# Kernel tuning notes

Measured on AMD Instinct MI355X. Metric: run time of the kernel, lower is better.

Reference implementation:

```python
import math
import jax, jax.numpy as jnp
import numpy as np

B, S, H, E, F = 4, 2048, 1024, 8, 2048
CAPACITY_FACTOR = 1.25


def setup_inputs() -> dict:
    key = jax.random.key(0)
    ks = jax.random.split(key, 5)
    x = jax.random.normal(ks[0], (B, S, H), dtype=jnp.float32)
    gate_w = jax.random.normal(ks[1], (H, E), dtype=jnp.float32) * 0.02
    w1 = jax.random.normal(ks[2], (E, H, F), dtype=jnp.float32) * 0.02
    w2 = jax.random.normal(ks[3], (E, F, H), dtype=jnp.float32) * 0.02
    w3 = jax.random.normal(ks[4], (E, H, F), dtype=jnp.float32) * 0.02
    return {"x": x, "gate_w": gate_w, "w1": w1, "w2": w2, "w3": w3}


def reference(x, gate_w, w1, w2, w3):
    b, s, h = x.shape
    T = b * s
    e = gate_w.shape[1]
    xf = x.reshape(T, h)                           # [T, H]
    logits = xf @ gate_w                           # [T, E]
    capacity = min(math.ceil(T / e * CAPACITY_FACTOR), T)
    # Expert-choice: each expert picks its top-`capacity` tokens.
    scores, idx = jax.lax.top_k(logits.T, capacity)  # both [E, C]
    # Per-expert softmax over the selected tokens (dim=0 of the column vector in torch == capacity axis here).
    weights = jax.nn.softmax(scores, axis=1)       # [E, C]
    gathered = xf[idx]                             # [E, C, H]
    # Grouped SwiGLU FFN
    a = jnp.einsum('ech,ehf->ecf', gathered, w1)
    g = jnp.einsum('ech,ehf->ecf', gathered, w3)
    hidden = jax.nn.silu(a) * g                    # [E, C, F]
    out_e = jnp.einsum('ecf,efh->ech', hidden, w2) # [E, C, H]
    out_e = out_e * weights[..., None]
    # Weighted scatter-add combine
    yf = jnp.zeros((T, h), dtype=x.dtype).at[idx.reshape(-1)].add(
        out_e.reshape(-1, h))
    return yf.reshape(b, s, h), jnp.float32(0.0)
```

## Files before the change

### kernel.cpp

```cpp
#include <hip/hip_runtime.h>
#include <stdint.h>

typedef unsigned short ushort_t;
typedef __bf16 bf16x8 __attribute__((ext_vector_type(8)));
typedef float f32x4 __attribute__((ext_vector_type(4)));

#define T_TOK 8192
#define HDIM  1024
#define EXP   8
#define FDIM  2048
#define CAP   1280

__device__ __forceinline__ unsigned short f2b(float f) {
  unsigned u = __float_as_uint(f);
  u = (u + 0x7fffu + ((u >> 16) & 1u)) >> 16;
  return (unsigned short)u;
}
__device__ __forceinline__ unsigned pk2(unsigned short lo, unsigned short hi) {
  return (unsigned)lo | ((unsigned)hi << 16);
}
__device__ __forceinline__ unsigned map_u(float f) {
  unsigned u = __float_as_uint(f);
  return (u & 0x80000000u) ? ~u : (u | 0x80000000u);
}
__device__ __forceinline__ float unmap_f(unsigned m) {
  unsigned u = (m & 0x80000000u) ? (m ^ 0x80000000u) : ~m;
  return __uint_as_float(u);
}
__device__ __forceinline__ void gl_lds16(const void* g, void* l) {
  __builtin_amdgcn_global_load_lds((__attribute__((address_space(1))) void*)g,
                                   (__attribute__((address_space(3))) void*)l,
                                   16, 0, 0);
}

__global__ void __launch_bounds__(256) gate_cast_k(
    const float* __restrict__ x, const float* __restrict__ gw,
    float* __restrict__ logitsT, ushort_t* __restrict__ xb)
{
  int wave = threadIdx.x >> 6, lane = threadIdx.x & 63;
  int t = blockIdx.x * 4 + wave;
  const float* xr = x + (size_t)t * HDIM;
  ushort_t* xbr = xb + (size_t)t * HDIM;
  float acc[8];
#pragma unroll
  for (int i = 0; i < 8; ++i) acc[i] = 0.f;
#pragma unroll
  for (int i = 0; i < 16; ++i) {
    int h = i * 64 + lane;
    float xv = xr[h];
    xbr[h] = f2b(xv);
    const float4* g4 = (const float4*)(gw + (size_t)h * EXP);
    float4 lo = g4[0], hi = g4[1];
    acc[0] += xv * lo.x; acc[1] += xv * lo.y; acc[2] += xv * lo.z; acc[3] += xv * lo.w;
    acc[4] += xv * hi.x; acc[5] += xv * hi.y; acc[6] += xv * hi.z; acc[7] += xv * hi.w;
  }
#pragma unroll
  for (int off = 32; off > 0; off >>= 1) {
#pragma unroll
    for (int i = 0; i < 8; ++i) acc[i] += __shfl_xor(acc[i], off, 64);
  }
  if (lane == 0) {
#pragma unroll
    for (int i = 0; i < 8; ++i) logitsT[(size_t)i * T_TOK + t] = acc[i];
  }
}

__global__ void __launch_bounds__(256) select_k(
    const float* __restrict__ logitsT,
    unsigned* __restrict__ thr, int* __restrict__ needo, unsigned* __restrict__ umax)
{
  __shared__ int hist[256];
  __shared__ int ssum[256];
  __shared__ unsigned s_pref;
  __shared__ int s_rem;
  __shared__ unsigned smx[4];
  int e = blockIdx.x, tid = threadIdx.x;
  const float* base = logitsT + (size_t)e * T_TOK;

  unsigned m[32];
  unsigned mmax = 0;
#pragma unroll
  for (int i = 0; i < 32; ++i) {
    m[i] = map_u(base[tid + i * 256]);
    mmax = m[i] > mmax ? m[i] : mmax;
  }
#pragma unroll
  for (int off = 32; off > 0; off >>= 1) {
    unsigned o = __shfl_xor(mmax, off, 64);
    mmax = o > mmax ? o : mmax;
  }
  int lane = tid & 63, wv = tid >> 6;
  if (lane == 0) smx[wv] = mmax;
  if (tid == 0) { s_pref = 0; s_rem = CAP; }
  __syncthreads();
  if (tid == 0) {
    unsigned a = smx[0] > smx[1] ? smx[0] : smx[1];
    unsigned b = smx[2] > smx[3] ? smx[2] : smx[3];
    umax[e] = a > b ? a : b;
  }

  for (int r = 0; r < 4; ++r) {
    hist[tid] = 0;
    __syncthreads();
    unsigned pref = s_pref;
    int rem = s_rem;
    int shift = 24 - 8 * r;
#pragma unroll
    for (int i = 0; i < 32; ++i) {
      unsigned u = m[i];
      bool ok = (r == 0) || ((u >> (shift + 8)) == (pref >> (shift + 8)));
      if (ok) atomicAdd(&hist[(u >> shift) & 255], 1);
    }
    __syncthreads();
    ssum[tid] = hist[tid];
    __syncthreads();
    for (int st = 1; st < 256; st <<= 1) {
      int add = (tid + st < 256) ? ssum[tid + st] : 0;
      __syncthreads();
      ssum[tid] += add;
      __syncthreads();
    }
    int above = (tid < 255) ? ssum[tid + 1] : 0;
    if (ssum[tid] >= rem && above < rem) {
      s_pref = pref | ((unsigned)tid << shift);
      s_rem = rem - above;
    }
    __syncthreads();
  }
  if (tid == 0) { thr[e] = s_pref; needo[e] = s_rem; }
}

__global__ void __launch_bounds__(256) emit_k(
    const float* __restrict__ logitsT,
    const unsigned* __restrict__ thr, const int* __restrict__ needv,
    const unsigned* __restrict__ umaxv,
    int* __restrict__ idxo, float* __restrict__ exo,
    int* __restrict__ cnt, int* __restrict__ tie, float* __restrict__ expsum,
    int* __restrict__ tok_cnt, int* __restrict__ tok_ent)
{
  int t = blockIdx.x * 256 + threadIdx.x;
  int lane = threadIdx.x & 63;
  int lc = 0;
  int ents[8];
#pragma unroll
  for (int e = 0; e < EXP; ++e) {
    float f = logitsT[(size_t)e * T_TOK + t];
    unsigned u = map_u(f);
    unsigned te = thr[e];
    float fm = unmap_f(umaxv[e]);
    float v = __expf(f - fm);
    bool sel = u > te;
    unsigned long long mask = __ballot(sel);
    int nsel = __popcll(mask);
    int base = 0;
    if (lane == 0 && nsel) base = atomicAdd(&cnt[e], nsel);
    base = __shfl(base, 0, 64);
    int slot = -1;
    if (sel) slot = base + __popcll(mask & ((1ull << lane) - 1ull));
    if (u == te) {
      int k = atomicAdd(&tie[e], 1);
      if (k < needv[e]) {
        slot = atomicAdd(&cnt[e], 1);
        atomicAdd(&expsum[e], v);
      }
    }
    if (slot >= 0) {
      idxo[e * CAP + slot] = t;
      exo[e * CAP + slot] = v;
      ents[lc++] = (e << 16) | slot;
    }
    float vs = sel ? v : 0.f;
#pragma unroll
    for (int off = 32; off > 0; off >>= 1) vs += __shfl_xor(vs, off, 64);
    if (lane == 0 && vs != 0.f) atomicAdd(&expsum[e], vs);
  }
  tok_cnt[t] = lc;
  for (int i = 0; i < lc; ++i) tok_ent[t * 8 + i] = ents[i];
}

__global__ void __launch_bounds__(256) transpose3_k(
    const float* __restrict__ w1, const float* __restrict__ w3, const float* __restrict__ w2,
    ushort_t* __restrict__ w1t, ushort_t* __restrict__ w3t, ushort_t* __restrict__ w2t)
{
  __shared__ float tile[64][65];
  int b = blockIdx.x;
  const float* in; ushort_t* out; int R, Cc;
  if (b < 4096)      { in = w1; out = w1t; R = HDIM; Cc = FDIM; }
  else if (b < 8192) { in = w3; out = w3t; R = HDIM; Cc = FDIM; b -= 4096; }
  else               { in = w2; out = w2t; R = FDIM; Cc = HDIM; b -= 8192; }
  int tilesC = Cc >> 6;
  int tilesPer = (R >> 6) * tilesC;
  int e = b / tilesPer;
  int tb = b - e * tilesPer;
  int rt = tb / tilesC, ct = tb - rt * tilesC;
  const float* src = in + (size_t)e * R * Cc;
  ushort_t* dst = out + (size_t)e * R * Cc;
  int tr = threadIdx.x >> 4, tc = threadIdx.x & 15;
#pragma unroll
  for (int it = 0; it < 4; ++it) {
    int r = (rt << 6) + (it << 4) + tr;
    int c = (ct << 6) + (tc << 2);
    float4 v = *(const float4*)(src + (size_t)r * Cc + c);
    tile[(it << 4) + tr][(tc << 2) + 0] = v.x;
    tile[(it << 4) + tr][(tc << 2) + 1] = v.y;
    tile[(it << 4) + tr][(tc << 2) + 2] = v.z;
    tile[(it << 4) + tr][(tc << 2) + 3] = v.w;
  }
  __syncthreads();
#pragma unroll
  for (int it = 0; it < 4; ++it) {
    int cl = (it << 4) + tr;
    int rl = tc << 2;
    unsigned lo = pk2(f2b(tile[rl + 0][cl]), f2b(tile[rl + 1][cl]));
    unsigned hi = pk2(f2b(tile[rl + 2][cl]), f2b(tile[rl + 3][cl]));
    unsigned long long v = (unsigned long long)lo | ((unsigned long long)hi << 32);
    *(unsigned long long*)(dst + (size_t)((ct << 6) + cl) * R + (rt << 6) + rl) = v;
  }
}

#define G1_STAGE(BB) \
  gl_lds16(pA0, lds + (BB)*12288 + (size_t)tid*8); \
  gl_lds16(pA1, lds + (BB)*12288 + 4096 + (size_t)tid*8); \
  gl_lds16(pB , lds + (BB)*12288 + 8192 + (size_t)tid*8);

#define G1_ITER(CB, PB, VM, PREF) { \
  asm volatile("s_waitcnt vmcnt(" VM ")" ::: "memory"); \
  __builtin_amdgcn_s_barrier(); \
  if (PREF) { G1_STAGE(PB); pA0 += 32; pA1 += 32; pB += 32; } \
  bf16x8 af[4], b1v[2], b3v[2]; \
  _Pragma("unroll") \
  for (int mi = 0; mi < 4; ++mi) af[mi] = *(const bf16x8*)(lds + (CB)*12288 + aoff[mi]); \
  _Pragma("unroll") \
  for (int nj = 0; nj < 2; ++nj) { \
    b1v[nj] = *(const bf16x8*)(lds + (CB)*12288 + b1off[nj]); \
    b3v[nj] = *(const bf16x8*)(lds + (CB)*12288 + b1off[nj] + 2048); } \
  __builtin_amdgcn_s_setprio(1); \
  _Pragma("unroll") \
  for (int mi = 0; mi < 4; ++mi) \
    _Pragma("unroll") \
    for (int nj = 0; nj < 2; ++nj) { \
      acc1[mi][nj] = __builtin_amdgcn_mfma_f32_16x16x32_bf16(af[mi], b1v[nj], acc1[mi][nj], 0, 0, 0); \
      acc3[mi][nj] = __builtin_amdgcn_mfma_f32_16x16x32_bf16(af[mi], b3v[nj], acc3[mi][nj], 0, 0, 0); } \
  __builtin_amdgcn_s_setprio(0); \
}

__global__ void __launch_bounds__(512) gemm1_swiglu_k(
    const ushort_t* __restrict__ xb,
    const ushort_t* __restrict__ w1t,
    const ushort_t* __restrict__ w3t,
    const int* __restrict__ idx,
    ushort_t* __restrict__ hidden)
{
  int b = blockIdx.x;
  int ft = b & 31; int t1 = b >> 5; int mt = t1 % 5; int e = t1 / 5;
  int f0 = ft * 64;

  __shared__ __bf16 lds[3 * 12288];

  int tid = threadIdx.x;
  int lane = tid & 63, wave = tid >> 6;
  int wm = wave >> 1;
  int wn = wave & 1;
  int l15 = lane & 15, quad = lane >> 4;

  int srow = tid >> 2;
  int chunk = tid & 3;
  int s_sw = (srow & 3) ^ ((srow >> 2) & 3);
  int g_chunk = ((chunk ^ s_sw) * 8);

  const int* idxe = idx + e * CAP + mt * 256;
  int tok0 = idxe[srow];
  int tok1 = idxe[srow + 128];
  const ushort_t* pA0 = xb + (size_t)tok0 * HDIM + g_chunk;
  const ushort_t* pA1 = xb + (size_t)tok1 * HDIM + g_chunk;
  const ushort_t* pB = (srow < 64)
      ? (w1t + ((size_t)e * FDIM + f0 + srow) * HDIM + g_chunk)
      : (w3t + ((size_t)e * FDIM + f0 + (srow - 64)) * HDIM + g_chunk);

  int aoff[4], b1off[2];
#pragma unroll
  for (int mi = 0; mi < 4; ++mi) {
    int R = wm * 64 + mi * 16 + l15;
    int sw = (R & 3) ^ ((R >> 2) & 3);
    aoff[mi] = R * 32 + ((quad ^ sw) * 8);
  }
#pragma unroll
  for (int nj = 0; nj < 2; ++nj) {
    int r1 = wn * 32 + nj * 16 + l15;
    int sw = (r1 & 3) ^ ((r1 >> 2) & 3);
    b1off[nj] = 8192 + r1 * 32 + ((quad ^ sw) * 8);
  }

  f32x4 acc1[4][2], acc3[4][2];
#pragma unroll
  for (int i = 0; i < 4; ++i)
#pragma unroll
    for (int j = 0; j < 2; ++j) {
      acc1[i][j] = (f32x4){0.f, 0.f, 0.f, 0.f};
      acc3[i][j] = (f32x4){0.f, 0.f, 0.f, 0.f};
    }

  G1_STAGE(0); pA0 += 32; pA1 += 32; pB += 32;
  G1_STAGE(1); pA0 += 32; pA1 += 32; pB += 32;

  for (int it = 0; it < 10; ++it) {
    G1_ITER(0, 2, "3", 1)
    G1_ITER(1, 0, "3", 1)
    G1_ITER(2, 1, "3", 1)
  }
  G1_ITER(0, 0, "3", 0)
  G1_ITER(1, 0, "0", 0)

  ushort_t* hb = hidden + ((size_t)e * CAP + mt * 256) * FDIM + f0;
#pragma unroll
  for (int mi = 0; mi < 4; ++mi)
#pragma unroll
    for (int nj = 0; nj < 2; ++nj)
#pragma unroll
      for (int r = 0; r < 4; ++r) {
        int row = wm * 64 + mi * 16 + quad * 4 + r;
        int col = wn * 32 + nj * 16 + l15;
        float v1 = acc1[mi][nj][r];
        float v3 = acc3[mi][nj][r];
        float s = (v1 / (1.f + __expf(-v1))) * v3;
        hb[(size_t)row * FDIM + col] = f2b(s);
      }
}

__global__ void __launch_bounds__(256) gemm2_k(
    const ushort_t* __restrict__ hidden,
    const ushort_t* __restrict__ w2t,
    const float* __restrict__ ex, const float* __restrict__ expsum,
    float* __restrict__ oute)
{
  int b = blockIdx.x;
  int nt = b & 7; int t1 = b >> 3; int mt = t1 % 10; int e = t1 / 10;

  __shared__ __bf16 Alds[2][128 * 64];
  __shared__ __bf16 Blds[2][128 * 64];
  __shared__ float wgts[128];

  int tid = threadIdx.x;
  int lane = tid & 63, wave = tid >> 6;
  int wm = wave & 1, wn = wave >> 1;
  int l15 = lane & 15, quad = lane >> 4;

  if (tid < 128) wgts[tid] = ex[e * CAP + mt * 128 + tid] / expsum[e];

  int kc = tid & 7;
  int r0 = tid >> 3;
  const ushort_t* a_ptr[4];
  const ushort_t* b_ptr[4];
#pragma unroll
  for (int j = 0; j < 4; ++j) {
    int row = r0 + j * 32;
    a_ptr[j] = hidden + ((size_t)e * CAP + mt * 128 + row) * FDIM + ((kc ^ (row & 7)) * 8);
    b_ptr[j] = w2t + ((size_t)e * HDIM + nt * 128 + row) * FDIM + ((kc ^ (row & 7)) * 8);
  }

  f32x4 acc[4][4];
#pragma unroll
  for (int i = 0; i < 4; ++i)
#pragma unroll
    for (int j = 0; j < 4; ++j) acc[i][j] = (f32x4){0.f, 0.f, 0.f, 0.f};

#pragma unroll
  for (int j = 0; j < 4; ++j) {
    gl_lds16(a_ptr[j], Alds[0] + ((size_t)tid + j * 256) * 8);
    gl_lds16(b_ptr[j], Blds[0] + ((size_t)tid + j * 256) * 8);
  }
#pragma unroll
  for (int j = 0; j < 4; ++j) { a_ptr[j] += 64; b_ptr[j] += 64; }
  __syncthreads();

  const int NT = FDIM / 64;
  int cur = 0;
  for (int kt = 0; kt < NT; ++kt) {
    const __bf16* Ac = Alds[cur];
    const __bf16* Bc = Blds[cur];
    __bf16* An = Alds[cur ^ 1];
    __bf16* Bn = Blds[cur ^ 1];

    if (kt + 1 < NT) {
#pragma unroll
      for (int j = 0; j < 4; ++j) {
        gl_lds16(a_ptr[j], An + ((size_t)tid + j * 256) * 8);
        gl_lds16(b_ptr[j], Bn + ((size_t)tid + j * 256) * 8);
      }
      if (kt + 2 < NT) {
#pragma unroll
        for (int j = 0; j < 4; ++j) { a_ptr[j] += 64; b_ptr[j] += 64; }
      }
    }

#pragma unroll
    for (int kh = 0; kh < 2; ++kh) {
      bf16x8 af[4], bf[4];
#pragma unroll
      for (int i = 0; i < 4; ++i) {
        int rowa = wm * 64 + i * 16 + l15;
        af[i] = *(const bf16x8*)(Ac + rowa * 64 + (((kh * 4 + quad) ^ (rowa & 7)) * 8));
        int rowb = wn * 64 + i * 16 + l15;
        bf[i] = *(const bf16x8*)(Bc + rowb * 64 + (((kh * 4 + quad) ^ (rowb & 7)) * 8));
      }
#pragma unroll
      for (int mi = 0; mi < 4; ++mi)
#pragma unroll
        for (int nj = 0; nj < 4; ++nj)
          acc[mi][nj] = __builtin_amdgcn_mfma_f32_16x16x32_bf16(af[mi], bf[nj], acc[mi][nj], 0, 0, 0);
    }
    __syncthreads();
    cur ^= 1;
  }

  float* ob = oute + ((size_t)e * CAP + mt * 128) * HDIM + nt * 128;
#pragma unroll
  for (int mi = 0; mi < 4; ++mi)
#pragma unroll
    for (int nj = 0; nj < 4; ++nj)
#pragma unroll
      for (int r = 0; r < 4; ++r) {
        int row = wm * 64 + mi * 16 + quad * 4 + r;
        int col = wn * 64 + nj * 16 + l15;
        ob[(size_t)row * HDIM + col] = acc[mi][nj][r] * wgts[row];
      }
}

__global__ void __launch_bounds__(256) combine_k(
    const float* __restrict__ oute,
    const int* __restrict__ tok_cnt, const int* __restrict__ tok_ent,
    float* __restrict__ y)
{
  int t = blockIdx.x;
  int c = threadIdx.x * 4;
  int n = tok_cnt[t];
  float4 acc = {0.f, 0.f, 0.f, 0.f};
  for (int i = 0; i < n; ++i) {
    int ent = tok_ent[t * 8 + i];
    int e = ent >> 16, slot = ent & 0xffff;
    float4 v = *(const float4*)(oute + (((size_t)e * CAP + slot) << 10) + c);
    acc.x += v.x; acc.y += v.y; acc.z += v.z; acc.w += v.w;
  }
  *(float4*)(y + ((size_t)t << 10) + c) = acc;
}

extern "C" void kernel_launch(void* const* d_in, const int* in_sizes, int n_in,
                              void* d_out, int out_size, void* d_ws, size_t ws_size,
                              hipStream_t stream)
{
  const float* x  = (const float*)d_in[0];
  const float* gw = (const float*)d_in[1];
  const float* w1 = (const float*)d_in[2];
  const float* w2 = (const float*)d_in[3];
  const float* w3 = (const float*)d_in[4];
  float* y = (float*)d_out;

  char* ws = (char*)d_ws;
  float*    logitsT = (float*)(ws + 0x0);
  int*      idx     = (int*)(ws + 0x40000);
  float*    exo     = (float*)(ws + 0x4A000);
  unsigned* thr    = (unsigned*)(ws + 0x54000);
  int*      need   = (int*)(ws + 0x54020);
  unsigned* umax   = (unsigned*)(ws + 0x54040);
  int*      cnt    = (int*)(ws + 0x54060);
  int*      tie    = (int*)(ws + 0x54080);
  float*    expsum = (float*)(ws + 0x540A0);
  int*      tok_cnt = (int*)(ws + 0x55000);
  int*      tok_ent = (int*)(ws + 0x5D000);
  ushort_t* xb     = (ushort_t*)(ws + 0xA0000);
  ushort_t* w1t    = (ushort_t*)(ws + 0x10A0000);
  ushort_t* w3t    = (ushort_t*)(ws + 0x30A0000);
  ushort_t* w2t    = (ushort_t*)(ws + 0x50A0000);
  ushort_t* hid    = (ushort_t*)(ws + 0x70A0000);
  float*    oute   = (float*)(ws + 0x10A0000);

  size_t yelems = (size_t)T_TOK * HDIM;
  if ((size_t)out_size > yelems)
    hipMemsetAsync((char*)d_out + yelems * 4, 0, ((size_t)out_size - yelems) * 4, stream);
  hipMemsetAsync(ws + 0x54000, 0, 256, stream);

  transpose3_k<<<3 * 4096, 256, 0, stream>>>(w1, w3, w2, w1t, w3t, w2t);
  gate_cast_k<<<T_TOK / 4, 256, 0, stream>>>(x, gw, logitsT, xb);
  select_k<<<EXP, 256, 0, stream>>>(logitsT, thr, need, umax);
  emit_k<<<T_TOK / 256, 256, 0, stream>>>(logitsT, thr, need, umax, idx, exo, cnt, tie, expsum, tok_cnt, tok_ent);
  gemm1_swiglu_k<<<EXP * 5 * 32, 512, 0, stream>>>(xb, w1t, w3t, idx, hid);
  gemm2_k<<<EXP * 10 * 8, 256, 0, stream>>>(hid, w2t, exo, expsum, oute);
  combine_k<<<T_TOK, 256, 0, stream>>>(oute, tok_cnt, tok_ent, y);
}
```

Measured before the change: 471.9 us.

## Triple-buffer gemm2 with 8 waves, remap block order, vectorize gate, per-wave histograms

gemm2 is rebuilt on gemm1's pattern: 512 threads, a 3-stage LDS ring with 32-wide K steps, explicit vmcnt waits and barriers, and setprio around the MFMA work. Both GEMMs remap blockIdx so consecutive blocks are spread across the XCDs. gate_cast now does float4 loads and packed bf16 stores, and select_k gives each wave its own histogram to cut atomic contention. These aim to hide load latency in the second GEMM and to improve cache locality, at the cost of more barriers per K step.

```diff
diff --git a/kernel.cpp b/kernel.cpp
--- a/kernel.cpp
+++ b/kernel.cpp
@@ -45,14 +45,22 @@
 #pragma unroll
   for (int i = 0; i < 8; ++i) acc[i] = 0.f;
 #pragma unroll
-  for (int i = 0; i < 16; ++i) {
-    int h = i * 64 + lane;
-    float xv = xr[h];
-    xbr[h] = f2b(xv);
-    const float4* g4 = (const float4*)(gw + (size_t)h * EXP);
-    float4 lo = g4[0], hi = g4[1];
-    acc[0] += xv * lo.x; acc[1] += xv * lo.y; acc[2] += xv * lo.z; acc[3] += xv * lo.w;
-    acc[4] += xv * hi.x; acc[5] += xv * hi.y; acc[6] += xv * hi.z; acc[7] += xv * hi.w;
+  for (int i = 0; i < 4; ++i) {
+    int h0 = i * 256 + lane * 4;
+    float4 xv = *(const float4*)(xr + h0);
+    unsigned lo = pk2(f2b(xv.x), f2b(xv.y));
+    unsigned hi = pk2(f2b(xv.z), f2b(xv.w));
+    *(unsigned long long*)(xbr + h0) = (unsigned long long)lo | ((unsigned long long)hi << 32);
+    float xs[4] = {xv.x, xv.y, xv.z, xv.w};
+#pragma unroll
+    for (int j = 0; j < 4; ++j) {
+      const float4* g4 = (const float4*)(gw + (size_t)(h0 + j) * EXP);
+      float4 glo = g4[0], ghi = g4[1];
+      acc[0] += xs[j] * glo.x; acc[1] += xs[j] * glo.y;
+      acc[2] += xs[j] * glo.z; acc[3] += xs[j] * glo.w;
+      acc[4] += xs[j] * ghi.x; acc[5] += xs[j] * ghi.y;
+      acc[6] += xs[j] * ghi.z; acc[7] += xs[j] * ghi.w;
+    }
   }
 #pragma unroll
   for (int off = 32; off > 0; off >>= 1) {
@@ -69,7 +77,7 @@
     const float* __restrict__ logitsT,
     unsigned* __restrict__ thr, int* __restrict__ needo, unsigned* __restrict__ umax)
 {
-  __shared__ int hist[256];
+  __shared__ int hist[4][256];
   __shared__ int ssum[256];
   __shared__ unsigned s_pref;
   __shared__ int s_rem;
@@ -100,7 +108,8 @@
   }
 
   for (int r = 0; r < 4; ++r) {
-    hist[tid] = 0;
+#pragma unroll
+    for (int w = 0; w < 4; ++w) hist[w][tid] = 0;
     __syncthreads();
     unsigned pref = s_pref;
     int rem = s_rem;
@@ -109,10 +118,10 @@
     for (int i = 0; i < 32; ++i) {
       unsigned u = m[i];
       bool ok = (r == 0) || ((u >> (shift + 8)) == (pref >> (shift + 8)));
-      if (ok) atomicAdd(&hist[(u >> shift) & 255], 1);
+      if (ok) atomicAdd(&hist[wv][(u >> shift) & 255], 1);
     }
     __syncthreads();
-    ssum[tid] = hist[tid];
+    ssum[tid] = hist[0][tid] + hist[1][tid] + hist[2][tid] + hist[3][tid];
     __syncthreads();
     for (int st = 1; st < 256; st <<= 1) {
       int add = (tid + st < 256) ? ssum[tid + st] : 0;
@@ -251,7 +260,8 @@
     const int* __restrict__ idx,
     ushort_t* __restrict__ hidden)
 {
-  int b = blockIdx.x;
+  int bb = blockIdx.x;
+  int b = (bb & 7) * 160 + (bb >> 3);
   int ft = b & 31; int t1 = b >> 5; int mt = t1 % 5; int e = t1 / 5;
   int f0 = ft * 64;
 
@@ -327,101 +337,99 @@
       }
 }
 
-__global__ void __launch_bounds__(256) gemm2_k(
+#define G2_STAGE(BB) \
+  gl_lds16(pA, lds2 + (BB)*8192 + (size_t)tid*8); \
+  gl_lds16(pB, lds2 + (BB)*8192 + 4096 + (size_t)tid*8);
+
+#define G2_ITER(CB, PB, VM, PREF) { \
+  asm volatile("s_waitcnt vmcnt(" VM ")" ::: "memory"); \
+  __builtin_amdgcn_s_barrier(); \
+  if (PREF) { G2_STAGE(PB); pA += 32; pB += 32; } \
+  bf16x8 af[4], bf[2]; \
+  _Pragma("unroll") \
+  for (int mi = 0; mi < 4; ++mi) af[mi] = *(const bf16x8*)(lds2 + (CB)*8192 + aoff[mi]); \
+  _Pragma("unroll") \
+  for (int nj = 0; nj < 2; ++nj) bf[nj] = *(const bf16x8*)(lds2 + (CB)*8192 + boff[nj]); \
+  __builtin_amdgcn_s_setprio(1); \
+  _Pragma("unroll") \
+  for (int mi = 0; mi < 4; ++mi) \
+    _Pragma("unroll") \
+    for (int nj = 0; nj < 2; ++nj) \
+      acc[mi][nj] = __builtin_amdgcn_mfma_f32_16x16x32_bf16(af[mi], bf[nj], acc[mi][nj], 0, 0, 0); \
+  __builtin_amdgcn_s_setprio(0); \
+}
+
+__global__ void __launch_bounds__(512) gemm2_k(
     const ushort_t* __restrict__ hidden,
     const ushort_t* __restrict__ w2t,
     const float* __restrict__ ex, const float* __restrict__ expsum,
     float* __restrict__ oute)
 {
-  int b = blockIdx.x;
+  int bb = blockIdx.x;
+  int b = (bb & 7) * 80 + (bb >> 3);
   int nt = b & 7; int t1 = b >> 3; int mt = t1 % 10; int e = t1 / 10;
 
-  __shared__ __bf16 Alds[2][128 * 64];
-  __shared__ __bf16 Blds[2][128 * 64];
+  __shared__ __bf16 lds2[3 * 8192];
   __shared__ float wgts[128];
 
   int tid = threadIdx.x;
   int lane = tid & 63, wave = tid >> 6;
-  int wm = wave & 1, wn = wave >> 1;
+  int wm = wave >> 2;
+  int wn = wave & 3;
   int l15 = lane & 15, quad = lane >> 4;
 
   if (tid < 128) wgts[tid] = ex[e * CAP + mt * 128 + tid] / expsum[e];
 
-  int kc = tid & 7;
-  int r0 = tid >> 3;
-  const ushort_t* a_ptr[4];
-  const ushort_t* b_ptr[4];
-#pragma unroll
-  for (int j = 0; j < 4; ++j) {
-    int row = r0 + j * 32;
-    a_ptr[j] = hidden + ((size_t)e * CAP + mt * 128 + row) * FDIM + ((kc ^ (row & 7)) * 8);
-    b_ptr[j] = w2t + ((size_t)e * HDIM + nt * 128 + row) * FDIM + ((kc ^ (row & 7)) * 8);
-  }
-
-  f32x4 acc[4][4];
+  int srow = tid >> 2;
+  int chunk = tid & 3;
+  int s_sw = (srow & 3) ^ ((srow >> 2) & 3);
+  int g_chunk = ((chunk ^ s_sw) * 8);
+
+  const ushort_t* pA = hidden + ((size_t)e * CAP + mt * 128 + srow) * FDIM + g_chunk;
+  const ushort_t* pB = w2t + ((size_t)e * HDIM + nt * 128 + srow) * FDIM + g_chunk;
+
+  int aoff[4], boff[2];
+#pragma unroll
+  for (int mi = 0; mi < 4; ++mi) {
+    int R = wm * 64 + mi * 16 + l15;
+    int sw = (R & 3) ^ ((R >> 2) & 3);
+    aoff[mi] = R * 32 + ((quad ^ sw) * 8);
+  }
+#pragma unroll
+  for (int nj = 0; nj < 2; ++nj) {
+    int r = wn * 32 + nj * 16 + l15;
+    int sw = (r & 3) ^ ((r >> 2) & 3);
+    boff[nj] = 4096 + r * 32 + ((quad ^ sw) * 8);
+  }
+
+  f32x4 acc[4][2];
 #pragma unroll
   for (int i = 0; i < 4; ++i)
 #pragma unroll
-    for (int j = 0; j < 4; ++j) acc[i][j] = (f32x4){0.f, 0.f, 0.f, 0.f};
-
-#pragma unroll
-  for (int j = 0; j < 4; ++j) {
-    gl_lds16(a_ptr[j], Alds[0] + ((size_t)tid + j * 256) * 8);
-    gl_lds16(b_ptr[j], Blds[0] + ((size_t)tid + j * 256) * 8);
-  }
-#pragma unroll
-  for (int j = 0; j < 4; ++j) { a_ptr[j] += 64; b_ptr[j] += 64; }
-  __syncthreads();
-
-  const int NT = FDIM / 64;
-  int cur = 0;
-  for (int kt = 0; kt < NT; ++kt) {
-    const __bf16* Ac = Alds[cur];
-    const __bf16* Bc = Blds[cur];
-    __bf16* An = Alds[cur ^ 1];
-    __bf16* Bn = Blds[cur ^ 1];
-
-    if (kt + 1 < NT) {
-#pragma unroll
-      for (int j = 0; j < 4; ++j) {
-        gl_lds16(a_ptr[j], An + ((size_t)tid + j * 256) * 8);
-        gl_lds16(b_ptr[j], Bn + ((size_t)tid + j * 256) * 8);
-      }
-      if (kt + 2 < NT) {
-#pragma unroll
-        for (int j = 0; j < 4; ++j) { a_ptr[j] += 64; b_ptr[j] += 64; }
-      }
-    }
-
-#pragma unroll
-    for (int kh = 0; kh < 2; ++kh) {
-      bf16x8 af[4], bf[4];
-#pragma unroll
-      for (int i = 0; i < 4; ++i) {
-        int rowa = wm * 64 + i * 16 + l15;
-        af[i] = *(const bf16x8*)(Ac + rowa * 64 + (((kh * 4 + quad) ^ (rowa & 7)) * 8));
-        int rowb = wn * 64 + i * 16 + l15;
-        bf[i] = *(const bf16x8*)(Bc + rowb * 64 + (((kh * 4 + quad) ^ (rowb & 7)) * 8));
-      }
-#pragma unroll
-      for (int mi = 0; mi < 4; ++mi)
-#pragma unroll
-        for (int nj = 0; nj < 4; ++nj)
-          acc[mi][nj] = __builtin_amdgcn_mfma_f32_16x16x32_bf16(af[mi], bf[nj], acc[mi][nj], 0, 0, 0);
-    }
-    __syncthreads();
-    cur ^= 1;
-  }
+    for (int j = 0; j < 2; ++j) acc[i][j] = (f32x4){0.f, 0.f, 0.f, 0.f};
+
+  G2_STAGE(0); pA += 32; pB += 32;
+  G2_STAGE(1); pA += 32; pB += 32;
+
+  for (int it = 0; it < 20; ++it) {
+    G2_ITER(0, 2, "2", 1)
+    G2_ITER(1, 0, "2", 1)
+    G2_ITER(2, 1, "2", 1)
+  }
+  G2_ITER(0, 2, "2", 1)
+  G2_ITER(1, 0, "2", 1)
+  G2_ITER(2, 0, "2", 0)
+  G2_ITER(0, 0, "0", 0)
 
   float* ob = oute + ((size_t)e * CAP + mt * 128) * HDIM + nt * 128;
 #pragma unroll
   for (int mi = 0; mi < 4; ++mi)
 #pragma unroll
-    for (int nj = 0; nj < 4; ++nj)
+    for (int nj = 0; nj < 2; ++nj)
 #pragma unroll
       for (int r = 0; r < 4; ++r) {
         int row = wm * 64 + mi * 16 + quad * 4 + r;
-        int col = wn * 64 + nj * 16 + l15;
+        int col = wn * 32 + nj * 16 + l15;
         ob[(size_t)row * HDIM + col] = acc[mi][nj][r] * wgts[row];
       }
 }
@@ -484,6 +492,6 @@
   select_k<<<EXP, 256, 0, stream>>>(logitsT, thr, need, umax);
   emit_k<<<T_TOK / 256, 256, 0, stream>>>(logitsT, thr, need, umax, idx, exo, cnt, tie, expsum, tok_cnt, tok_ent);
   gemm1_swiglu_k<<<EXP * 5 * 32, 512, 0, stream>>>(xb, w1t, w3t, idx, hid);
-  gemm2_k<<<EXP * 10 * 8, 256, 0, stream>>>(hid, w2t, exo, expsum, oute);
+  gemm2_k<<<EXP * 10 * 8, 512, 0, stream>>>(hid, w2t, exo, expsum, oute);
   combine_k<<<T_TOK, 256, 0, stream>>>(oute, tok_cnt, tok_ent, y);
 }
```

Measured after the change: 468.9 us. Within noise of the previous version (-0.6%).
